# Kernel tuning notes

Hardware: AMD Instinct MI355X
Metric: run time of the kernel (lower is better)

Reference implementation:

```python
import jax, jax.numpy as jnp
import numpy as np

N_NODES = 100000
N_EDGES = 1600000
N_FEAT = 128
N_CLASSES = 64
K_HOPS = 2


def setup_inputs() -> dict:
    key = jax.random.key(0)
    k1, k2, k3 = jax.random.split(key, 3)
    x = jax.random.normal(k1, (N_NODES, N_FEAT), dtype=jnp.float32)
    edge_index = jax.random.randint(k2, (2, N_EDGES), 0, N_NODES, dtype=jnp.int64)
    # Linear layer params (PyG Linear: y = x @ W.T + b)
    lim = 1.0 / np.sqrt(N_FEAT)
    W = jax.random.uniform(k3, (N_CLASSES, N_FEAT), dtype=jnp.float32, minval=-lim, maxval=lim)
    b = jnp.zeros((N_CLASSES,), dtype=jnp.float32)
    return {"x": x, "edge_index": edge_index, "W": W, "b": b}


def _gcn_norm(edge_index, num_nodes):
    # Add self-loops with weight 1 (PyG gcn_norm default)
    loops = jnp.arange(num_nodes, dtype=edge_index.dtype)
    row = jnp.concatenate([edge_index[0], loops])
    col = jnp.concatenate([edge_index[1], loops])
    ew = jnp.ones(row.shape[0], dtype=jnp.float32)
    deg = jax.ops.segment_sum(ew, col, num_segments=num_nodes)
    dinv = jnp.where(deg > 0, jax.lax.rsqrt(deg), 0.0)
    norm = dinv[row] * ew * dinv[col]  # [E + N]
    return row, col, norm


def reference(x, edge_index, W, b):
    n = x.shape[0]
    row, col, norm = _gcn_norm(edge_index, n)
    # K rounds of normalized SpMM: out[col] += norm * x[row]
    for _ in range(K_HOPS):
        x = jax.ops.segment_sum(norm[:, None] * x[row], col, num_segments=n)
    # Final linear
    return x @ W.T + b
```

## Files before the change

kernel.cpp:

```cpp
#include <hip/hip_runtime.h>
#include <hip/hip_fp16.h>

#define NFEAT 128
#define NCLS  64
#define CPB   192
#define SCAP  3600
#define NBMAX 544
#define PCHUNK 8192

typedef _Float16 f16;
typedef __attribute__((ext_vector_type(8))) _Float16 f16x8;
typedef __attribute__((ext_vector_type(4))) float f32x4;

__global__ __launch_bounds__(256) void fat_k(const float* __restrict__ x,
                                             const float* __restrict__ W,
                                             const int* __restrict__ row,
                                             const int* __restrict__ col, int E,
                                             int* __restrict__ bcursor,
                                             int* __restrict__ ebuf,
                                             f16* __restrict__ u0,
                                             int n, int NB, int PB) {
    __shared__ union {
        struct { int ecol[PCHUNK]; int h[NBMAX]; int cur[NBMAX]; } p;
        __align__(16) f16 zbuf[4][16][64];
    } sh;
    int t = threadIdx.x;

    if ((int)blockIdx.x < PB) {
        int start = blockIdx.x * PCHUNK;
        int end   = min(start + PCHUNK, E);
        int cnt_c = end - start;
        for (int i = t; i < NB; i += 256) sh.p.h[i] = 0;
        for (int k = t; k < cnt_c; k += 256) sh.p.ecol[k] = col[start + k];
        __syncthreads();
        for (int k = t; k < cnt_c; k += 256)
            atomicAdd(&sh.p.h[sh.p.ecol[k] / CPB], 1);
        __syncthreads();
        for (int i = t; i < NB; i += 256)
            sh.p.cur[i] = i * SCAP + (sh.p.h[i] ? atomicAdd(&bcursor[i], sh.p.h[i]) : 0);
        __syncthreads();
        for (int k = t; k < cnt_c; k += 256) {
            int c = sh.p.ecol[k], b = c / CPB, cl = c - b * CPB;
            int pos = atomicAdd(&sh.p.cur[b], 1);
            if (pos < (b + 1) * SCAP)
                ebuf[pos] = row[start + k] | (cl << 17);
        }
        return;
    }

    int w = t >> 6, l = t & 63;
    int lr = l & 15;
    int lk = l >> 4;

    f16x8 bfrag[4][4];
#pragma unroll
    for (int ct = 0; ct < 4; ++ct)
#pragma unroll
        for (int m = 0; m < 4; ++m) {
            const float* wp = &W[(size_t)(ct * 16 + lr) * NFEAT + m * 32 + lk * 8];
            float4 w0 = *reinterpret_cast<const float4*>(wp);
            float4 w1 = *reinterpret_cast<const float4*>(wp + 4);
            f16x8 bb;
            bb[0] = (f16)w0.x; bb[1] = (f16)w0.y; bb[2] = (f16)w0.z; bb[3] = (f16)w0.w;
            bb[4] = (f16)w1.x; bb[5] = (f16)w1.y; bb[6] = (f16)w1.z; bb[7] = (f16)w1.w;
            bfrag[ct][m] = bb;
        }

    int nb = (blockIdx.x - PB) * 64 + w * 16;
    int arow = nb + lr;
    bool aok = arow < n;
    const float* xp = &x[(size_t)(aok ? arow : 0) * NFEAT + lk * 8];

    f32x4 acc[4];
#pragma unroll
    for (int ct = 0; ct < 4; ++ct) acc[ct] = (f32x4){0.f, 0.f, 0.f, 0.f};

#pragma unroll
    for (int m = 0; m < 4; ++m) {
        float4 x0 = make_float4(0.f, 0.f, 0.f, 0.f);
        float4 x1 = make_float4(0.f, 0.f, 0.f, 0.f);
        if (aok) {
            x0 = *reinterpret_cast<const float4*>(xp + m * 32);
            x1 = *reinterpret_cast<const float4*>(xp + m * 32 + 4);
        }
        f16x8 a;
        a[0] = (f16)x0.x; a[1] = (f16)x0.y; a[2] = (f16)x0.z; a[3] = (f16)x0.w;
        a[4] = (f16)x1.x; a[5] = (f16)x1.y; a[6] = (f16)x1.z; a[7] = (f16)x1.w;
#pragma unroll
        for (int ct = 0; ct < 4; ++ct)
            acc[ct] = __builtin_amdgcn_mfma_f32_16x16x32_f16(a, bfrag[ct][m], acc[ct], 0, 0, 0);
    }

#pragma unroll
    for (int ct = 0; ct < 4; ++ct)
#pragma unroll
        for (int r = 0; r < 4; ++r)
            sh.zbuf[w][lk * 4 + r][ct * 16 + lr] = (f16)acc[ct][r];
    __builtin_amdgcn_s_waitcnt(0);

    const uint4* zb = reinterpret_cast<const uint4*>(&sh.zbuf[w][0][0]);
    uint4 v0 = zb[l * 2], v1 = zb[l * 2 + 1];
    int node = nb + (l >> 2);
    if (node < n) {
        uint4* op = reinterpret_cast<uint4*>(&u0[(size_t)node * NCLS + (l & 3) * 16]);
        op[0] = v0; op[1] = v1;
    }
}

__global__ __launch_bounds__(256) void sort_k(const int* __restrict__ ebuf,
                                              const int* __restrict__ bcursor,
                                              const f16* __restrict__ u0,
                                              f16* __restrict__ z0,
                                              float* __restrict__ dinv,
                                              int2* __restrict__ pc,
                                              int* __restrict__ csr, int N) {
    __shared__ int sld[SCAP];
    __shared__ int h[CPB];
    __shared__ int cur[CPB];
    __shared__ int sc[256];
    __shared__ float ds[CPB];
    int b = blockIdx.x, t = threadIdx.x;
    int base = b * SCAP;
    int cntb = min(bcursor[b], SCAP);
    for (int i = t; i < CPB; i += 256) h[i] = 0;
    for (int j = t; j < cntb; j += 256) sld[j] = ebuf[base + j];
    __syncthreads();
    for (int j = t; j < cntb; j += 256)
        atomicAdd(&h[sld[j] >> 17], 1);
    __syncthreads();
    int v = (t < CPB) ? h[t] : 0;
    sc[t] = v;
    for (int off = 1; off < 256; off <<= 1) {
        __syncthreads();
        int a = (t >= off) ? sc[t - off] : 0;
        __syncthreads();
        sc[t] += a;
    }
    __syncthreads();
    if (t < CPB) {
        int c = b * CPB + t;
        int p = base + sc[t] - v;
        cur[t] = p;
        float d = rsqrtf((float)(v + 1));
        ds[t] = d;
        if (c < N) {
            pc[c] = make_int2(p, v);
            dinv[c] = d;
        }
    }
    __syncthreads();
    for (int j = t; j < cntb; j += 256) {
        int e = sld[j];
        int pos = atomicAdd(&cur[e >> 17], 1);
        csr[pos] = e & 0x1FFFF;
    }
    int nodes = min(CPB, N - b * CPB);
    if (nodes > 0) {
        const uint4* up = reinterpret_cast<const uint4*>(u0 + (size_t)b * CPB * NCLS);
        uint4* zp = reinterpret_cast<uint4*>(z0 + (size_t)b * CPB * NCLS);
        int tot = nodes * 8;
        for (int i = t; i < tot; i += 256) {
            float d = ds[i >> 3];
            uint4 vv = up[i];
            __half2* hv = reinterpret_cast<__half2*>(&vv);
#pragma unroll
            for (int k = 0; k < 4; ++k) {
                float2 f = __half22float2(hv[k]);
                hv[k] = __floats2half2_rn(f.x * d, f.y * d);
            }
            zp[i] = vv;
        }
    }
}

template <int FINAL>
__global__ __launch_bounds__(256) void spmm_k(const __half* __restrict__ zin,
                                              void* __restrict__ outp,
                                              const int2* __restrict__ pc,
                                              const float* __restrict__ dinv,
                                              const int* __restrict__ csr,
                                              const float* __restrict__ bias, int n) {
    int t = threadIdx.x;
    int lane = t & 63;
    int wid  = blockIdx.x * 4 + (t >> 6);
    wid = __builtin_amdgcn_readfirstlane(wid);
    if (wid >= n) return;

    int sub = lane >> 3;
    int cg  = (lane & 7) * 8;
    int2 se = pc[wid];
    int s = se.x, e = s + se.y;

    float a[8];
#pragma unroll
    for (int k = 0; k < 8; ++k) a[k] = 0.f;

#define ACCUM(u)                                                            \
    {                                                                       \
        __half2 t0 = *reinterpret_cast<const __half2*>(&u.x);               \
        __half2 t1 = *reinterpret_cast<const __half2*>(&u.y);               \
        __half2 t2 = *reinterpret_cast<const __half2*>(&u.z);               \
        __half2 t3 = *reinterpret_cast<const __half2*>(&u.w);               \
        float2 f0 = __half22float2(t0), f1 = __half22float2(t1);            \
        float2 f2 = __half22float2(t2), f3 = __half22float2(t3);            \
        a[0] += f0.x; a[1] += f0.y; a[2] += f1.x; a[3] += f1.y;             \
        a[4] += f2.x; a[5] += f2.y; a[6] += f3.x; a[7] += f3.y;             \
    }
#define GATHER(r) (*reinterpret_cast<const uint4*>(&zin[(size_t)(r) * NCLS + cg]))

    int j = s;
    while (e - j >= 32) {
        int r0 = csr[j + sub],      r1 = csr[j + 8 + sub];
        int r2 = csr[j + 16 + sub], r3 = csr[j + 24 + sub];
        uint4 g0 = GATHER(r0), g1 = GATHER(r1), g2 = GATHER(r2), g3 = GATHER(r3);
        ACCUM(g0); ACCUM(g1); ACCUM(g2); ACCUM(g3);
        j += 32;
    }
    int f = (e - j) >> 3;
    uint4 g0, g1, g2, g3;
    bool p = (j + f * 8 + sub) < e;
    if (f > 0) { int r = csr[j + sub];           g0 = GATHER(r); }
    if (f > 1) { int r = csr[j + 8 + sub];       g1 = GATHER(r); }
    if (f > 2) { int r = csr[j + 16 + sub];      g2 = GATHER(r); }
    if (p)     { int r = csr[j + f * 8 + sub];   g3 = GATHER(r); }
    if (f > 0) ACCUM(g0);
    if (f > 1) ACCUM(g1);
    if (f > 2) ACCUM(g2);
    if (p)     ACCUM(g3);

#pragma unroll
    for (int m = 8; m <= 32; m <<= 1)
#pragma unroll
        for (int k = 0; k < 8; ++k)
            a[k] += __shfl_xor(a[k], m, 64);

    uint4 sv = GATHER(wid);
    ACCUM(sv);
#undef GATHER
#undef ACCUM

    float d = dinv[wid];
    if (FINAL) {
        float* out = (float*)outp;
        float4 b0 = *reinterpret_cast<const float4*>(&bias[cg]);
        float4 b1 = *reinterpret_cast<const float4*>(&bias[cg + 4]);
        if (sub == 0) {
            float4 o0, o1;
            o0.x = fmaf(d, a[0], b0.x); o0.y = fmaf(d, a[1], b0.y);
            o0.z = fmaf(d, a[2], b0.z); o0.w = fmaf(d, a[3], b0.w);
            o1.x = fmaf(d, a[4], b1.x); o1.y = fmaf(d, a[5], b1.y);
            o1.z = fmaf(d, a[6], b1.z); o1.w = fmaf(d, a[7], b1.w);
            *reinterpret_cast<float4*>(&out[(size_t)wid * NCLS + cg])     = o0;
            *reinterpret_cast<float4*>(&out[(size_t)wid * NCLS + cg + 4]) = o1;
        }
    } else {
        __half* zo = (__half*)outp;
        float d2 = d * d;
        if (sub == 0) {
            __half2 h0 = __floats2half2_rn(d2 * a[0], d2 * a[1]);
            __half2 h1 = __floats2half2_rn(d2 * a[2], d2 * a[3]);
            __half2 h2 = __floats2half2_rn(d2 * a[4], d2 * a[5]);
            __half2 h3 = __floats2half2_rn(d2 * a[6], d2 * a[7]);
            uint4 pk;
            pk.x = *reinterpret_cast<unsigned int*>(&h0);
            pk.y = *reinterpret_cast<unsigned int*>(&h1);
            pk.z = *reinterpret_cast<unsigned int*>(&h2);
            pk.w = *reinterpret_cast<unsigned int*>(&h3);
            *reinterpret_cast<uint4*>(&zo[(size_t)wid * NCLS + cg]) = pk;
        }
    }
}

extern "C" void kernel_launch(void* const* d_in, const int* in_sizes, int n_in,
                              void* d_out, int out_size, void* d_ws, size_t ws_size,
                              hipStream_t stream) {
    const float* x  = (const float*)d_in[0];
    const int*   ei = (const int*)d_in[1];
    const float* W  = (const float*)d_in[2];
    const float* b  = (const float*)d_in[3];

    const int N = in_sizes[0] / NFEAT;
    const int E = in_sizes[1] / 2;
    const int* row = ei;
    const int* col = ei + E;
    const int NB = (N + CPB - 1) / CPB;
    if (NB > NBMAX) return;

    const int PB    = (E + PCHUNK - 1) / PCHUNK;
    const int PROJB = (N + 63) / 64;

    const size_t SLOTS = (size_t)NB * SCAP;
    f16*   u0      = (f16*)d_ws;
    f16*   z0      = u0 + (size_t)N * NCLS;
    int*   ebuf    = (int*)(z0 + (size_t)N * NCLS);
    int*   csr     = ebuf + SLOTS;
    float* dinv    = (float*)(csr + SLOTS);
    int2*  pc      = (int2*)(dinv + N);
    int*   bcursor = (int*)(pc + N);

    size_t needed = (size_t)N * NCLS * 2 * 2
                  + (SLOTS * 2 + (size_t)N * 3 + (size_t)NB) * 4;
    if (ws_size < needed) return;

    hipMemsetAsync(bcursor, 0, (size_t)NB * 4, stream);
    fat_k<<<PB + PROJB, 256, 0, stream>>>(x, W, row, col, E, bcursor, ebuf, u0, N, NB, PB);
    sort_k<<<NB, 256, 0, stream>>>(ebuf, bcursor, u0, z0, dinv, pc, csr, N);

    f16* z1 = u0;
    spmm_k<0><<<(N + 3) / 4, 256, 0, stream>>>((const __half*)z0, (void*)z1, pc, dinv, csr, b, N);
    spmm_k<1><<<(N + 3) / 4, 256, 0, stream>>>((const __half*)z1, d_out,     pc, dinv, csr, b, N);
}
```

Before: 239.4 us.

## Locally sort edge partitions before writing buckets; widen blocks; hoist SpMM self loads

The partition phase now builds a per-block exclusive prefix over bucket counts, scatters packed edges into a locally sorted shared buffer, then writes them to global buckets in order, finding each edge's bucket by binary search. This makes the global bucket writes contiguous instead of scattered. Partition, projection and sort kernels move to 512-thread blocks, with projection covering 128 nodes per block. The SpMM kernel issues the self-row gather and dinv load earlier so they overlap with the neighbour gathers. In exchange it adds a scan, an extra shared pass, a binary search per edge and larger shared memory use, which can lower occupancy.

Result: no change. 242.9 us (+1.4%).

```diff
diff --git a/kernel.cpp b/kernel.cpp
--- a/kernel.cpp
+++ b/kernel.cpp
@@ -12,7 +12,7 @@
 typedef __attribute__((ext_vector_type(8))) _Float16 f16x8;
 typedef __attribute__((ext_vector_type(4))) float f32x4;
 
-__global__ __launch_bounds__(256) void fat_k(const float* __restrict__ x,
+__global__ __launch_bounds__(512) void fat_k(const float* __restrict__ x,
                                              const float* __restrict__ W,
                                              const int* __restrict__ row,
                                              const int* __restrict__ col, int E,
@@ -21,8 +21,15 @@
                                              f16* __restrict__ u0,
                                              int n, int NB, int PB) {
     __shared__ union {
-        struct { int ecol[PCHUNK]; int h[NBMAX]; int cur[NBMAX]; } p;
-        __align__(16) f16 zbuf[4][16][64];
+        struct {
+            int sorted[PCHUNK];
+            int hist[NBMAX];
+            int sps[NBMAX + 1];
+            int cur[NBMAX];
+            int gbase[NBMAX];
+            int sc[512];
+        } p;
+        __align__(16) f16 zbuf[8][16][64];
     } sh;
     int t = threadIdx.x;
 
@@ -30,20 +37,48 @@
         int start = blockIdx.x * PCHUNK;
         int end   = min(start + PCHUNK, E);
         int cnt_c = end - start;
-        for (int i = t; i < NB; i += 256) sh.p.h[i] = 0;
-        for (int k = t; k < cnt_c; k += 256) sh.p.ecol[k] = col[start + k];
-        __syncthreads();
-        for (int k = t; k < cnt_c; k += 256)
-            atomicAdd(&sh.p.h[sh.p.ecol[k] / CPB], 1);
-        __syncthreads();
-        for (int i = t; i < NB; i += 256)
-            sh.p.cur[i] = i * SCAP + (sh.p.h[i] ? atomicAdd(&bcursor[i], sh.p.h[i]) : 0);
-        __syncthreads();
-        for (int k = t; k < cnt_c; k += 256) {
-            int c = sh.p.ecol[k], b = c / CPB, cl = c - b * CPB;
-            int pos = atomicAdd(&sh.p.cur[b], 1);
-            if (pos < (b + 1) * SCAP)
-                ebuf[pos] = row[start + k] | (cl << 17);
+        for (int i = t; i < NB; i += 512) sh.p.hist[i] = 0;
+        __syncthreads();
+        for (int k = t; k < cnt_c; k += 512)
+            atomicAdd(&sh.p.hist[col[start + k] / CPB], 1);
+        __syncthreads();
+        int i0 = 2 * t, i1 = 2 * t + 1;
+        int a0 = (i0 < NB) ? sh.p.hist[i0] : 0;
+        int a1 = (i1 < NB) ? sh.p.hist[i1] : 0;
+        sh.p.sc[t] = a0 + a1;
+        for (int off = 1; off < 512; off <<= 1) {
+            __syncthreads();
+            int a = (t >= off) ? sh.p.sc[t - off] : 0;
+            __syncthreads();
+            sh.p.sc[t] += a;
+        }
+        __syncthreads();
+        int excl = sh.p.sc[t] - a0 - a1;
+        if (i0 <= NB) sh.p.sps[i0] = excl;
+        if (i1 <= NB) sh.p.sps[i1] = excl + a0;
+        if (t == 511) sh.p.sps[NB] = sh.p.sc[511];
+        __syncthreads();
+        for (int i = t; i < NB; i += 512) {
+            int hv = sh.p.hist[i];
+            sh.p.gbase[i] = hv ? atomicAdd(&bcursor[i], hv) : 0;
+            sh.p.cur[i]   = sh.p.sps[i];
+        }
+        __syncthreads();
+        for (int k = t; k < cnt_c; k += 512) {
+            int c = col[start + k], b = c / CPB, cl = c - b * CPB;
+            int lpos = atomicAdd(&sh.p.cur[b], 1);
+            sh.p.sorted[lpos] = row[start + k] | (cl << 17);
+        }
+        __syncthreads();
+        for (int k = t; k < cnt_c; k += 512) {
+            int lo = 0, hi = NB;
+            while (hi - lo > 1) {
+                int mid = (lo + hi) >> 1;
+                if (sh.p.sps[mid] <= k) lo = mid; else hi = mid;
+            }
+            int off = sh.p.gbase[lo] + (k - sh.p.sps[lo]);
+            if (off < SCAP)
+                ebuf[lo * SCAP + off] = sh.p.sorted[k];
         }
         return;
     }
@@ -66,7 +101,7 @@
             bfrag[ct][m] = bb;
         }
 
-    int nb = (blockIdx.x - PB) * 64 + w * 16;
+    int nb = (blockIdx.x - PB) * 128 + w * 16;
     int arow = nb + lr;
     bool aok = arow < n;
     const float* xp = &x[(size_t)(aok ? arow : 0) * NFEAT + lk * 8];
@@ -107,7 +142,7 @@
     }
 }
 
-__global__ __launch_bounds__(256) void sort_k(const int* __restrict__ ebuf,
+__global__ __launch_bounds__(512) void sort_k(const int* __restrict__ ebuf,
                                               const int* __restrict__ bcursor,
                                               const f16* __restrict__ u0,
                                               f16* __restrict__ z0,
@@ -117,24 +152,24 @@
     __shared__ int sld[SCAP];
     __shared__ int h[CPB];
     __shared__ int cur[CPB];
-    __shared__ int sc[256];
+    __shared__ int sc[512];
     __shared__ float ds[CPB];
     int b = blockIdx.x, t = threadIdx.x;
     int base = b * SCAP;
     int cntb = min(bcursor[b], SCAP);
-    for (int i = t; i < CPB; i += 256) h[i] = 0;
-    for (int j = t; j < cntb; j += 256) sld[j] = ebuf[base + j];
+    if (t < CPB) h[t] = 0;
+    for (int j = t; j < cntb; j += 512) sld[j] = ebuf[base + j];
     __syncthreads();
-    for (int j = t; j < cntb; j += 256)
+    for (int j = t; j < cntb; j += 512)
         atomicAdd(&h[sld[j] >> 17], 1);
     __syncthreads();
     int v = (t < CPB) ? h[t] : 0;
     sc[t] = v;
     for (int off = 1; off < 256; off <<= 1) {
         __syncthreads();
-        int a = (t >= off) ? sc[t - off] : 0;
-        __syncthreads();
-        sc[t] += a;
+        int a = (t >= off && t < 256) ? sc[t - off] : 0;
+        __syncthreads();
+        if (t < 256) sc[t] += a;
     }
     __syncthreads();
     if (t < CPB) {
@@ -149,7 +184,7 @@
         }
     }
     __syncthreads();
-    for (int j = t; j < cntb; j += 256) {
+    for (int j = t; j < cntb; j += 512) {
         int e = sld[j];
         int pos = atomicAdd(&cur[e >> 17], 1);
         csr[pos] = e & 0x1FFFF;
@@ -159,7 +194,7 @@
         const uint4* up = reinterpret_cast<const uint4*>(u0 + (size_t)b * CPB * NCLS);
         uint4* zp = reinterpret_cast<uint4*>(z0 + (size_t)b * CPB * NCLS);
         int tot = nodes * 8;
-        for (int i = t; i < tot; i += 256) {
+        for (int i = t; i < tot; i += 512) {
             float d = ds[i >> 3];
             uint4 vv = up[i];
             __half2* hv = reinterpret_cast<__half2*>(&vv);
@@ -188,7 +223,12 @@
 
     int sub = lane >> 3;
     int cg  = (lane & 7) * 8;
+
+#define GATHER(r) (*reinterpret_cast<const uint4*>(&zin[(size_t)(r) * NCLS + cg]))
+
     int2 se = pc[wid];
+    uint4 sv = GATHER(wid);
+    float d = dinv[wid];
     int s = se.x, e = s + se.y;
 
     float a[8];
@@ -206,7 +246,6 @@
         a[0] += f0.x; a[1] += f0.y; a[2] += f1.x; a[3] += f1.y;             \
         a[4] += f2.x; a[5] += f2.y; a[6] += f3.x; a[7] += f3.y;             \
     }
-#define GATHER(r) (*reinterpret_cast<const uint4*>(&zin[(size_t)(r) * NCLS + cg]))
 
     int j = s;
     while (e - j >= 32) {
@@ -234,12 +273,10 @@
         for (int k = 0; k < 8; ++k)
             a[k] += __shfl_xor(a[k], m, 64);
 
-    uint4 sv = GATHER(wid);
     ACCUM(sv);
 #undef GATHER
 #undef ACCUM
 
-    float d = dinv[wid];
     if (FINAL) {
         float* out = (float*)outp;
         float4 b0 = *reinterpret_cast<const float4*>(&bias[cg]);
@@ -287,7 +324,7 @@
     if (NB > NBMAX) return;
 
     const int PB    = (E + PCHUNK - 1) / PCHUNK;
-    const int PROJB = (N + 63) / 64;
+    const int PROJB = (N + 127) / 128;
 
     const size_t SLOTS = (size_t)NB * SCAP;
     f16*   u0      = (f16*)d_ws;
@@ -303,8 +340,8 @@
     if (ws_size < needed) return;
 
     hipMemsetAsync(bcursor, 0, (size_t)NB * 4, stream);
-    fat_k<<<PB + PROJB, 256, 0, stream>>>(x, W, row, col, E, bcursor, ebuf, u0, N, NB, PB);
-    sort_k<<<NB, 256, 0, stream>>>(ebuf, bcursor, u0, z0, dinv, pc, csr, N);
+    fat_k<<<PB + PROJB, 512, 0, stream>>>(x, W, row, col, E, bcursor, ebuf, u0, N, NB, PB);
+    sort_k<<<NB, 512, 0, stream>>>(ebuf, bcursor, u0, z0, dinv, pc, csr, N);
 
     f16* z1 = u0;
     spmm_k<0><<<(N + 3) / 4, 256, 0, stream>>>((const __half*)z0, (void*)z1, pc, dinv, csr, b, N);
```
